# Kernel optimization log

Hardware: AMD Instinct MI355X
Metric: run time of the kernel (lower is better)

The kernel has to match this reference:

```python
import jax, jax.numpy as jnp
import numpy as np

B, T, E, H, V, F_IN = 128, 64, 512, 512, 10000, 2048


def setup_inputs() -> dict:
    key = jax.random.key(0)
    ks = jax.random.split(key, 16)
    u = lambda k, s, a: jax.random.uniform(k, s, jnp.float32, -a, a)
    n = lambda k, s, std: jax.random.normal(k, s, jnp.float32) * std
    return {
        "features": jax.random.normal(ks[0], (B, F_IN), jnp.float32),
        "captions": jax.random.randint(ks[1], (B, T), 0, V),
        "h0": jax.random.normal(ks[2], (B, H), jnp.float32),
        "lengths": T,
        "embed_W": u(ks[3], (V, E), 0.1),
        "fc_W": n(ks[4], (E, F_IN), 0.02),
        "fc_b": jnp.zeros((E,), jnp.float32),
        "bn_gamma": jnp.ones((E,), jnp.float32),
        "bn_beta": jnp.zeros((E,), jnp.float32),
        "attn_W": n(ks[5], (H, 2 * H), 0.02),
        "attn_b": jnp.zeros((H,), jnp.float32),
        "comb_W": n(ks[6], (H, 2 * H), 0.02),
        "comb_b": jnp.zeros((H,), jnp.float32),
        "gru_Wih": u(ks[7], (3 * H, E), 1.0 / np.sqrt(H)),
        "gru_Whh": u(ks[8], (3 * H, H), 1.0 / np.sqrt(H)),
        "gru_bih": u(ks[9], (3 * H,), 1.0 / np.sqrt(H)),
        "gru_bhh": u(ks[10], (3 * H,), 1.0 / np.sqrt(H)),
        "out_W": u(ks[11], (V, H), 0.1),
        "out_b": jnp.zeros((V,), jnp.float32),
    }


def _forward(features, captions, h0, lengths, embed_W, fc_W, fc_b, bn_gamma,
             bn_beta, attn_W, attn_b, comb_W, comb_b, gru_Wih, gru_Whh,
             gru_bih, gru_bhh, out_W, out_b):
    # fc + BatchNorm1d (training mode: batch statistics, eps=1e-5)
    f = features @ fc_W.T + fc_b                      # [B, E]
    mu = jnp.mean(f, axis=0)
    var = jnp.var(f, axis=0)
    feats = bn_gamma * (f - mu) / jnp.sqrt(var + 1e-5) + bn_beta  # [B, E]

    # embeddings = cat(features, embed(captions)); loop uses first T steps
    emb = embed_W[captions]                           # [B, T, E]
    x_seq = jnp.concatenate([feats[:, None, :], emb], axis=1)[:, :lengths]
    x_seq = jnp.swapaxes(x_seq, 0, 1)                 # [T, B, E]

    def step(hx, x):
        aw = jax.nn.softmax(jnp.concatenate([x, hx], 1) @ attn_W.T + attn_b,
                            axis=1)                   # [B, H]
        applied = feats * aw                          # [B, E]
        inp = jnp.concatenate([x, applied], 1) @ comb_W.T + comb_b  # [B, H]
        gx = inp @ gru_Wih.T + gru_bih                # [B, 3H]
        gh = hx @ gru_Whh.T + gru_bhh                 # [B, 3H]
        xr, xz, xn = jnp.split(gx, 3, axis=1)
        hr, hz, hn = jnp.split(gh, 3, axis=1)
        r = jax.nn.sigmoid(xr + hr)
        z = jax.nn.sigmoid(xz + hz)
        nt = jnp.tanh(xn + r * hn)
        h = (1.0 - z) * nt + z * hx
        return h, h

    _, hs = jax.lax.scan(step, h0, x_seq)             # hs: [T, B, H]
    hiddens = jnp.swapaxes(hs, 0, 1)                  # [B, T, H]
    # pack_padded_sequence with equal lengths -> time-major flatten
    packed = hs.reshape(lengths * hiddens.shape[0], -1)  # [T*B, H]
    logits = packed @ out_W.T + out_b                 # [T*B, V]
    return jax.nn.log_softmax(logits, axis=1), hiddens


def reference(features, captions, h0, lengths, embed_W, fc_W, fc_b, bn_gamma,
              bn_beta, attn_W, attn_b, comb_W, comb_b, gru_Wih, gru_Whh,
              gru_bih, gru_bhh, out_W, out_b):
    return _forward(features, captions, h0, lengths, embed_W, fc_W, fc_b,
                    bn_gamma, bn_beta, attn_W, attn_b, comb_W, comb_b,
                    gru_Wih, gru_Whh, gru_bih, gru_bhh, out_W, out_b)
```

## Files before the change

### kernel.cpp

```cpp
#include <hip/hip_runtime.h>

#define BB 128
#define TT 64
#define EE 512
#define HH 512
#define VV 10000
#define FIN 2048

typedef __attribute__((ext_vector_type(4))) float f32x4_t;
typedef __attribute__((ext_vector_type(8))) short s16x8_t;

__device__ __forceinline__ unsigned short f2bf(float x) {
    unsigned int u = __float_as_uint(x);
    unsigned int r = (u + 0x7fffu + ((u >> 16) & 1u)) >> 16;
    return (unsigned short)r;
}

__global__ __launch_bounds__(256) void gemm32(
    const float* __restrict__ A, int lda,
    const float* __restrict__ Bw, int ldb,
    float* __restrict__ C, int ldc, int K,
    const float* __restrict__ bias)
{
    __shared__ float As[32][34];
    __shared__ float Bs[32][34];
    const int tx = threadIdx.x, ty = threadIdx.y;
    const int tid = ty * 16 + tx;
    const int m0 = blockIdx.y * 32, n0 = blockIdx.x * 32;
    const int lr = tid >> 3, lc = (tid & 7) << 2;
    const float* ap = A + (size_t)(m0 + lr) * lda + lc;
    const float* bp = Bw + (size_t)(n0 + lr) * ldb + lc;
    float c00 = 0.f, c01 = 0.f, c10 = 0.f, c11 = 0.f;
    for (int kc = 0; kc < K; kc += 32) {
        float4 av = *(const float4*)(ap + kc);
        float4 bv = *(const float4*)(bp + kc);
        __syncthreads();
        As[lc + 0][lr] = av.x; As[lc + 1][lr] = av.y;
        As[lc + 2][lr] = av.z; As[lc + 3][lr] = av.w;
        Bs[lc + 0][lr] = bv.x; Bs[lc + 1][lr] = bv.y;
        Bs[lc + 2][lr] = bv.z; Bs[lc + 3][lr] = bv.w;
        __syncthreads();
#pragma unroll
        for (int kk = 0; kk < 32; kk++) {
            float2 a = *(const float2*)&As[kk][2 * ty];
            float2 b = *(const float2*)&Bs[kk][2 * tx];
            c00 = fmaf(a.x, b.x, c00); c01 = fmaf(a.x, b.y, c01);
            c10 = fmaf(a.y, b.x, c10); c11 = fmaf(a.y, b.y, c11);
        }
    }
    float cc[2][2] = {{c00, c01}, {c10, c11}};
    const int row = m0 + 2 * ty, col = n0 + 2 * tx;
#pragma unroll
    for (int i = 0; i < 2; i++)
#pragma unroll
        for (int j = 0; j < 2; j++)
            C[(size_t)(row + i) * ldc + col + j] = cc[i][j] + bias[col + j];
}

__global__ __launch_bounds__(256) void gemm128(
    const unsigned short* __restrict__ A, const unsigned short* __restrict__ Bw,
    float* __restrict__ C, int N, int K,
    const float* __restrict__ bias,
    const float* __restrict__ base, int ldbase, int mode)
{
    __shared__ __align__(16) unsigned short As[128 * 32];
    __shared__ __align__(16) unsigned short Bs[128 * 32];
    const int tid = threadIdx.x;
    const int lane = tid & 63, wave = tid >> 6;
    const int bm = blockIdx.y * 128, bn = blockIdx.x * 128;
    const int wm = (wave & 1) * 64, wn = (wave >> 1) * 64;
    const int sr = tid >> 2, sc = (tid & 3) * 8;
    const int m16 = lane & 15, q = lane >> 4;

    f32x4_t acc[4][4];
#pragma unroll
    for (int i = 0; i < 4; i++)
#pragma unroll
        for (int j = 0; j < 4; j++)
            acc[i][j] = (f32x4_t){0.f, 0.f, 0.f, 0.f};

    for (int kc = 0; kc < K; kc += 32) {
        uint4 a0 = *(const uint4*)(A + (size_t)(bm + sr) * K + kc + sc);
        uint4 a1 = *(const uint4*)(A + (size_t)(bm + 64 + sr) * K + kc + sc);
        uint4 b0, b1;
        int rb0 = bn + sr, rb1 = bn + 64 + sr;
        if (rb0 < N) b0 = *(const uint4*)(Bw + (size_t)rb0 * K + kc + sc);
        else { b0.x = 0; b0.y = 0; b0.z = 0; b0.w = 0; }
        if (rb1 < N) b1 = *(const uint4*)(Bw + (size_t)rb1 * K + kc + sc);
        else { b1.x = 0; b1.y = 0; b1.z = 0; b1.w = 0; }
        __syncthreads();
        *(uint4*)(&As[sr * 32 + sc]) = a0;
        *(uint4*)(&As[(sr + 64) * 32 + sc]) = a1;
        *(uint4*)(&Bs[sr * 32 + sc]) = b0;
        *(uint4*)(&Bs[(sr + 64) * 32 + sc]) = b1;
        __syncthreads();

        s16x8_t af[4], bf[4];
#pragma unroll
        for (int i = 0; i < 4; i++) {
            af[i] = *(const s16x8_t*)(&As[(wm + i * 16 + m16) * 32 + q * 8]);
            bf[i] = *(const s16x8_t*)(&Bs[(wn + i * 16 + m16) * 32 + q * 8]);
        }
#pragma unroll
        for (int i = 0; i < 4; i++)
#pragma unroll
            for (int j = 0; j < 4; j++)
                acc[i][j] = __builtin_amdgcn_mfma_f32_16x16x32_bf16(af[i], bf[j], acc[i][j], 0, 0, 0);
    }

#pragma unroll
    for (int i = 0; i < 4; i++)
#pragma unroll
        for (int j = 0; j < 4; j++) {
            int gr = bm + wm + i * 16 + q * 4;
            int gc = bn + wn + j * 16 + m16;
            if (gc < N) {
                if (mode == 0) {
                    float addc = bias ? bias[gc] : 0.f;
#pragma unroll
                    for (int rr = 0; rr < 4; rr++) {
                        float v = acc[i][j][rr] + addc;
                        if (base) v += base[(size_t)(gr + rr) * ldbase + gc];
                        C[(size_t)(gr + rr) * N + gc] = v;
                    }
                } else {
#pragma unroll
                    for (int rr = 0; rr < 4; rr++) {
                        int r = gr + rr;
                        float v = acc[i][j][rr];
                        v += (gc < 512) ? base[r * 512 + gc] : bias[gc - 512];
                        C[(size_t)r * N + gc] = v;
                    }
                }
            }
        }
}

__global__ __launch_bounds__(256) void gemm64(
    const unsigned short* __restrict__ A, const unsigned short* __restrict__ Bw,
    float* __restrict__ C, int N, int K,
    const float* __restrict__ bias,
    const float* __restrict__ base, int ldbase, int mode)
{
    __shared__ __align__(16) unsigned short As[64 * 32];
    __shared__ __align__(16) unsigned short Bs[64 * 32];
    const int tid = threadIdx.x;
    const int lane = tid & 63, wave = tid >> 6;
    const int bm = blockIdx.y * 64, bn = blockIdx.x * 64;
    const int wm = (wave & 1) * 32, wn = (wave >> 1) * 32;
    const int sr = tid >> 2, sc = (tid & 3) * 8;
    const int m16 = lane & 15, q = lane >> 4;

    f32x4_t acc[2][2];
#pragma unroll
    for (int i = 0; i < 2; i++)
#pragma unroll
        for (int j = 0; j < 2; j++)
            acc[i][j] = (f32x4_t){0.f, 0.f, 0.f, 0.f};

    for (int kc = 0; kc < K; kc += 32) {
        uint4 a0 = *(const uint4*)(A + (size_t)(bm + sr) * K + kc + sc);
        uint4 b0 = *(const uint4*)(Bw + (size_t)(bn + sr) * K + kc + sc);
        __syncthreads();
        *(uint4*)(&As[sr * 32 + sc]) = a0;
        *(uint4*)(&Bs[sr * 32 + sc]) = b0;
        __syncthreads();

        s16x8_t af[2], bf[2];
#pragma unroll
        for (int i = 0; i < 2; i++) {
            af[i] = *(const s16x8_t*)(&As[(wm + i * 16 + m16) * 32 + q * 8]);
            bf[i] = *(const s16x8_t*)(&Bs[(wn + i * 16 + m16) * 32 + q * 8]);
        }
#pragma unroll
        for (int i = 0; i < 2; i++)
#pragma unroll
            for (int j = 0; j < 2; j++)
                acc[i][j] = __builtin_amdgcn_mfma_f32_16x16x32_bf16(af[i], bf[j], acc[i][j], 0, 0, 0);
    }

#pragma unroll
    for (int i = 0; i < 2; i++)
#pragma unroll
        for (int j = 0; j < 2; j++) {
            int gr = bm + wm + i * 16 + q * 4;
            int gc = bn + wn + j * 16 + m16;
            if (mode == 0) {
                float addc = bias ? bias[gc] : 0.f;
#pragma unroll
                for (int rr = 0; rr < 4; rr++) {
                    float v = acc[i][j][rr] + addc;
                    if (base) v += base[(size_t)(gr + rr) * ldbase + gc];
                    C[(size_t)(gr + rr) * N + gc] = v;
                }
            } else {
#pragma unroll
                for (int rr = 0; rr < 4; rr++) {
                    int r = gr + rr;
                    float v = acc[i][j][rr];
                    v += (gc < 512) ? base[r * 512 + gc] : bias[gc - 512];
                    C[(size_t)r * N + gc] = v;
                }
            }
        }
}

__global__ __launch_bounds__(128) void bn_kernel(
    const float* __restrict__ f, const float* __restrict__ gamma,
    const float* __restrict__ beta, float* __restrict__ feats)
{
    int e = blockIdx.x, b = threadIdx.x;
    float v = f[b * EE + e];
    __shared__ float s1[128], s2[128];
    s1[b] = v; s2[b] = v * v;
    __syncthreads();
    for (int s = 64; s > 0; s >>= 1) {
        if (b < s) { s1[b] += s1[b + s]; s2[b] += s2[b + s]; }
        __syncthreads();
    }
    float mu = s1[0] * (1.f / 128.f);
    float var = s2[0] * (1.f / 128.f) - mu * mu;
    float inv = 1.f / sqrtf(var + 1e-5f);
    feats[b * EE + e] = gamma[e] * (v - mu) * inv + beta[e];
}

__global__ void build_x_bf16(const float* __restrict__ feats, const float* __restrict__ embW,
                             const int* __restrict__ cap, unsigned short* __restrict__ Xb)
{
    int id = blockIdx.x * 256 + threadIdx.x;
    int e4 = id & 127;
    int rem = id >> 7;
    int b = rem & 127;
    int t = rem >> 7;
    const float4* src;
    if (t == 0) src = (const float4*)(feats + b * EE) + e4;
    else        src = (const float4*)(embW + (size_t)cap[b * TT + t - 1] * EE) + e4;
    float4 v = *src;
    ushort4 o;
    o.x = f2bf(v.x); o.y = f2bf(v.y); o.z = f2bf(v.z); o.w = f2bf(v.w);
    ((ushort4*)Xb)[(size_t)(t * BB + b) * 128 + e4] = o;
}

__global__ void cvt_bf16(const float* __restrict__ src, unsigned short* __restrict__ dst, int n)
{
    int i = blockIdx.x * 256 + threadIdx.x;
    if (i < n) dst[i] = f2bf(src[i]);
}

__global__ void pack_attn_wx(const float* __restrict__ attnW, unsigned short* __restrict__ dst)
{
    int i = blockIdx.x * 256 + threadIdx.x;
    int n = i >> 9, e = i & 511;
    dst[i] = f2bf(attnW[n * 1024 + e]);
}

__global__ void pack_cxt(const float* __restrict__ combW, unsigned short* __restrict__ dst)
{
    int i = blockIdx.x * 256 + threadIdx.x;
    int e = i >> 9, n = i & 511;
    dst[i] = f2bf(combW[n * 1024 + e]);
}

__global__ void pack_wat(const float* __restrict__ combW, unsigned short* __restrict__ dst)
{
    int i = blockIdx.x * 256 + threadIdx.x;
    int m = i >> 9, n = i & 511;
    dst[i] = f2bf(combW[n * 1024 + 512 + m]);
}

__global__ void pack_wcat_bf(const float* __restrict__ attnW, const float* __restrict__ Whh,
                             unsigned short* __restrict__ dst)
{
    int i = blockIdx.x * 256 + threadIdx.x;
    int j = i >> 9, k = i & 511;
    dst[i] = f2bf((j < 512) ? attnW[j * 1024 + 512 + k]
                            : Whh[(size_t)(j - 512) * 512 + k]);
}

__global__ void bias2_kernel(const float* __restrict__ Wih, const float* __restrict__ comb_b,
                             const float* __restrict__ bih, float* __restrict__ bias2)
{
    int j = blockIdx.x, lane = threadIdx.x;
    float s = 0.f;
    for (int n = lane; n < 512; n += 64) s += Wih[(size_t)j * 512 + n] * comb_b[n];
    for (int o = 32; o > 0; o >>= 1) s += __shfl_down(s, o);
    if (lane == 0) bias2[j] = bih[j] + s;
}

__global__ __launch_bounds__(256) void softmax_applied(
    const float* __restrict__ AB, const float* __restrict__ feats,
    unsigned short* __restrict__ APPb)
{
    int b = blockIdx.x, tid = threadIdx.x;
    const float* L = AB + b * 2048;
    float v0 = L[tid], v1 = L[tid + 256];
    __shared__ float red[256];
    red[tid] = fmaxf(v0, v1);
    __syncthreads();
    for (int s = 128; s > 0; s >>= 1) {
        if (tid < s) red[tid] = fmaxf(red[tid], red[tid + s]);
        __syncthreads();
    }
    float mx = red[0];
    __syncthreads();
    float e0 = __expf(v0 - mx), e1 = __expf(v1 - mx);
    red[tid] = e0 + e1;
    __syncthreads();
    for (int s = 128; s > 0; s >>= 1) {
        if (tid < s) red[tid] += red[tid + s];
        __syncthreads();
    }
    float inv = 1.f / red[0];
    APPb[b * 512 + tid]       = f2bf(feats[b * 512 + tid] * e0 * inv);
    APPb[b * 512 + tid + 256] = f2bf(feats[b * 512 + tid + 256] * e1 * inv);
}

__global__ __launch_bounds__(256) void gru_gate(
    const float* __restrict__ GX, const float* __restrict__ AB,
    const float* __restrict__ hprev, float* __restrict__ hs_t,
    unsigned short* __restrict__ hsb_t)
{
    int i = blockIdx.x * 256 + threadIdx.x;
    int b = i >> 9, n = i & 511;
    float xr = GX[b * 1536 + n];
    float xz = GX[b * 1536 + 512 + n];
    float xn = GX[b * 1536 + 1024 + n];
    float hr = AB[b * 2048 + 512 + n];
    float hz = AB[b * 2048 + 1024 + n];
    float hn = AB[b * 2048 + 1536 + n];
    float r = 1.f / (1.f + __expf(-(xr + hr)));
    float z = 1.f / (1.f + __expf(-(xz + hz)));
    float nt = tanhf(xn + r * hn);
    float h = (1.f - z) * nt + z * hprev[i];
    hs_t[i] = h;
    hsb_t[i] = f2bf(h);
}

__global__ __launch_bounds__(256) void row_lse(const float* __restrict__ C, float* __restrict__ lse)
{
    int row = blockIdx.x, tid = threadIdx.x;
    const float* p = C + (size_t)row * VV;
    float m = -1e30f;
    for (int i = tid; i < VV; i += 256) m = fmaxf(m, p[i]);
    __shared__ float red[256];
    red[tid] = m;
    __syncthreads();
    for (int s = 128; s > 0; s >>= 1) {
        if (tid < s) red[tid] = fmaxf(red[tid], red[tid + s]);
        __syncthreads();
    }
    float mx = red[0];
    __syncthreads();
    float ssum = 0.f;
    for (int i = tid; i < VV; i += 256) ssum += __expf(p[i] - mx);
    red[tid] = ssum;
    __syncthreads();
    for (int s = 128; s > 0; s >>= 1) {
        if (tid < s) red[tid] += red[tid + s];
        __syncthreads();
    }
    if (tid == 0) lse[row] = mx + logf(red[0]);
}

__global__ void sub_lse(float* __restrict__ C, const float* __restrict__ lse)
{
    int i = blockIdx.x * 256 + threadIdx.x;
    float l = lse[i / 2500];
    float4 v = ((float4*)C)[i];
    v.x -= l; v.y -= l; v.z -= l; v.w -= l;
    ((float4*)C)[i] = v;
}

__global__ void copy_hiddens(const float* __restrict__ HS, float* __restrict__ out)
{
    int id = blockIdx.x * 256 + threadIdx.x;
    int h4 = id & 127;
    int t = (id >> 7) & 63;
    int b = id >> 13;
    ((float4*)out)[id] = ((const float4*)HS)[t * 16384 + b * 128 + h4];
}

extern "C" void kernel_launch(void* const* d_in, const int* in_sizes, int n_in,
                              void* d_out, int out_size, void* d_ws, size_t ws_size,
                              hipStream_t stream)
{
    const float* features = (const float*)d_in[0];
    const int*   captions = (const int*)d_in[1];
    const float* h0       = (const float*)d_in[2];
    const float* embed_W  = (const float*)d_in[4];
    const float* fc_W     = (const float*)d_in[5];
    const float* fc_b     = (const float*)d_in[6];
    const float* bn_gamma = (const float*)d_in[7];
    const float* bn_beta  = (const float*)d_in[8];
    const float* attn_W   = (const float*)d_in[9];
    const float* attn_b   = (const float*)d_in[10];
    const float* comb_W   = (const float*)d_in[11];
    const float* comb_b   = (const float*)d_in[12];
    const float* gru_Wih  = (const float*)d_in[13];
    const float* gru_Whh  = (const float*)d_in[14];
    const float* gru_bih  = (const float*)d_in[15];
    const float* gru_bhh  = (const float*)d_in[16];
    const float* out_W    = (const float*)d_in[17];
    const float* out_b    = (const float*)d_in[18];
    float* dout = (float*)d_out;

    float* w      = (float*)d_ws;
    float* f      = w;
    float* feats  = w + 65536;
    float* Lx     = w + 131072;
    float* GxX    = w + 4325376;
    float* HS     = w + 16908288;
    float* W2     = w + 21102592;
    float* W_ac   = w + 21889024;
    float* AB     = w + 22675456;
    float* GX     = w + 22937600;
    float* bias2  = w + 23134208;
    float* lse    = w + 23135744;
    unsigned short* u      = (unsigned short*)(w + 23143936);
    unsigned short* Xb     = u;
    unsigned short* attnWxb= u + 4194304;
    unsigned short* Wihb   = u + 4456448;
    unsigned short* CxTb   = u + 5242880;
    unsigned short* WaTb   = u + 5505024;
    unsigned short* Wcatb  = u + 5767168;
    unsigned short* W2b    = u + 6815744;
    unsigned short* W_acb  = u + 7602176;
    unsigned short* outWb  = u + 8388608;
    unsigned short* HSb    = u + 13508608;
    unsigned short* APPb   = u + 17702912;
    unsigned short* h0b    = u + 17768448;

    dim3 blk2(16, 16);

    gemm32<<<dim3(16, 4), blk2, 0, stream>>>(features, FIN, fc_W, FIN, f, EE, FIN, fc_b);
    bn_kernel<<<512, 128, 0, stream>>>(f, bn_gamma, bn_beta, feats);
    cvt_bf16<<<256, 256, 0, stream>>>(h0, h0b, BB * HH);
    build_x_bf16<<<4096, 256, 0, stream>>>(feats, embed_W, captions, Xb);
    pack_attn_wx<<<1024, 256, 0, stream>>>(attn_W, attnWxb);
    pack_cxt<<<1024, 256, 0, stream>>>(comb_W, CxTb);
    pack_wat<<<1024, 256, 0, stream>>>(comb_W, WaTb);
    pack_wcat_bf<<<4096, 256, 0, stream>>>(attn_W, gru_Whh, Wcatb);
    cvt_bf16<<<3072, 256, 0, stream>>>(gru_Wih, Wihb, 1536 * 512);
    cvt_bf16<<<20000, 256, 0, stream>>>(out_W, outWb, VV * HH);
    bias2_kernel<<<1536, 64, 0, stream>>>(gru_Wih, comb_b, gru_bih, bias2);

    gemm128<<<dim3(4, 64), 256, 0, stream>>>(Xb, attnWxb, Lx, 512, 512,
                                             attn_b, nullptr, 0, 0);
    gemm64<<<dim3(8, 24), 256, 0, stream>>>(Wihb, CxTb, W2, 512, 512,
                                            nullptr, nullptr, 0, 0);
    cvt_bf16<<<3072, 256, 0, stream>>>(W2, W2b, 1536 * 512);
    gemm128<<<dim3(12, 64), 256, 0, stream>>>(Xb, W2b, GxX, 1536, 512,
                                              bias2, nullptr, 0, 0);
    gemm64<<<dim3(8, 24), 256, 0, stream>>>(Wihb, WaTb, W_ac, 512, 512,
                                            nullptr, nullptr, 0, 0);
    cvt_bf16<<<3072, 256, 0, stream>>>(W_ac, W_acb, 1536 * 512);

    for (int t = 0; t < TT; t++) {
        const unsigned short* hb = (t == 0) ? h0b : (HSb + (size_t)(t - 1) * BB * HH);
        const float* hprev = (t == 0) ? h0 : (HS + (size_t)(t - 1) * BB * HH);
        gemm64<<<dim3(32, 2), 256, 0, stream>>>(hb, Wcatb, AB, 2048, 512,
                                                gru_bhh, Lx + (size_t)t * BB * HH, 512, 1);
        softmax_applied<<<128, 256, 0, stream>>>(AB, feats, APPb);
        gemm64<<<dim3(24, 2), 256, 0, stream>>>(APPb, W_acb, GX, 1536, 512,
                                                nullptr, GxX + (size_t)t * BB * 1536, 1536, 0);
        gru_gate<<<256, 256, 0, stream>>>(GX, AB, hprev,
                                          HS + (size_t)t * BB * HH,
                                          HSb + (size_t)t * BB * HH);
    }

    gemm128<<<dim3(79, 64), 256, 0, stream>>>(HSb, outWb, dout, VV, 512,
                                              out_b, nullptr, 0, 0);
    row_lse<<<8192, 256, 0, stream>>>(dout, lse);
    sub_lse<<<80000, 256, 0, stream>>>(dout, lse);
    copy_hiddens<<<4096, 256, 0, stream>>>(HS, dout + (size_t)TT * BB * VV);
}
```

Measured before the change: 2.738 ms.

## Fuse GRU recurrence into persistent kernel with grid barriers and fuse log-softmax

Replaces the 256 per-timestep launches (GEMM, softmax, GEMM, gate) with one persistent 48-block kernel. The kernel keeps the recurrent weights resident in swizzled LDS and separates phases with atomic grid barriers. The GRU gate is fused into the second GEMM's epilogue. The separate row_lse and sub_lse passes become one log-softmax kernel that caches each row in LDS. This removes launch overhead and repeated weight reloads, at the cost of spin-barrier latency, low occupancy, and relying on all 48 blocks being co-resident.

```diff
diff --git a/kernel.cpp b/kernel.cpp
--- a/kernel.cpp
+++ b/kernel.cpp
@@ -7,6 +7,10 @@
 #define VV 10000
 #define FIN 2048
 
+#define NBLK 48
+#define NA 32
+#define NC 16
+
 typedef __attribute__((ext_vector_type(4))) float f32x4_t;
 typedef __attribute__((ext_vector_type(8))) short s16x8_t;
 
@@ -14,6 +18,10 @@
     unsigned int u = __float_as_uint(x);
     unsigned int r = (u + 0x7fffu + ((u >> 16) & 1u)) >> 16;
     return (unsigned short)r;
+}
+
+__device__ __forceinline__ int swz(int row, int kb) {
+    return row * 1024 + (kb ^ ((row & 7) << 4));
 }
 
 __global__ __launch_bounds__(256) void gemm32(
@@ -287,88 +295,233 @@
     if (lane == 0) bias2[j] = bih[j] + s;
 }
 
-__global__ __launch_bounds__(256) void softmax_applied(
-    const float* __restrict__ AB, const float* __restrict__ feats,
-    unsigned short* __restrict__ APPb)
-{
-    int b = blockIdx.x, tid = threadIdx.x;
-    const float* L = AB + b * 2048;
-    float v0 = L[tid], v1 = L[tid + 256];
-    __shared__ float red[256];
-    red[tid] = fmaxf(v0, v1);
+__global__ void zero_u32(unsigned int* __restrict__ p) { *p = 0u; }
+
+__device__ __forceinline__ void gbar(unsigned int* cnt, unsigned int tgt)
+{
     __syncthreads();
-    for (int s = 128; s > 0; s >>= 1) {
-        if (tid < s) red[tid] = fmaxf(red[tid], red[tid + s]);
-        __syncthreads();
-    }
-    float mx = red[0];
+    if (threadIdx.x == 0) {
+        __threadfence();
+        __hip_atomic_fetch_add(cnt, 1u, __ATOMIC_ACQ_REL, __HIP_MEMORY_SCOPE_AGENT);
+        while (__hip_atomic_load(cnt, __ATOMIC_RELAXED, __HIP_MEMORY_SCOPE_AGENT) < tgt)
+            __builtin_amdgcn_s_sleep(2);
+        __threadfence();
+    }
     __syncthreads();
-    float e0 = __expf(v0 - mx), e1 = __expf(v1 - mx);
-    red[tid] = e0 + e1;
+}
+
+__global__ __launch_bounds__(256) void recurrence(
+    const unsigned short* __restrict__ Wcatb,
+    const unsigned short* __restrict__ W_acb,
+    const unsigned short* __restrict__ h0b,
+    const float* __restrict__ h0,
+    const float* __restrict__ Lx,
+    const float* __restrict__ GxX,
+    const float* __restrict__ feats,
+    const float* __restrict__ bhh,
+    float* __restrict__ AB,
+    unsigned short* __restrict__ APPb,
+    float* __restrict__ HS,
+    unsigned short* __restrict__ HSb,
+    unsigned int* __restrict__ barcnt)
+{
+    __shared__ __align__(16) unsigned char smem[96 * 1024];
+    const int tid = threadIdx.x;
+    const int bid = blockIdx.x;
+    const int lane = tid & 63, wave = tid >> 6;
+    const int m16 = lane & 15, q = lane >> 4;
+
+    if (bid < NA) {
+        const uint4* src = (const uint4*)(Wcatb + (size_t)bid * 64 * 512);
+#pragma unroll
+        for (int it = 0; it < 16; it++) {
+            int idx = it * 256 + tid;
+            int r = idx >> 6, sl = idx & 63;
+            *(uint4*)(smem + swz(r, sl * 16)) = src[idx];
+        }
+    } else {
+        const int n0c = (bid - NA) * 32;
+#pragma unroll
+        for (int it = 0; it < 24; it++) {
+            int idx = it * 256 + tid;
+            int r = idx >> 6, sl = idx & 63;
+            int p = r >> 5, rr = r & 31;
+            *(uint4*)(smem + swz(r, sl * 16)) =
+                ((const uint4*)(W_acb + (size_t)(p * 512 + n0c + rr) * 512))[sl];
+        }
+    }
     __syncthreads();
-    for (int s = 128; s > 0; s >>= 1) {
-        if (tid < s) red[tid] += red[tid + s];
-        __syncthreads();
-    }
-    float inv = 1.f / red[0];
-    APPb[b * 512 + tid]       = f2bf(feats[b * 512 + tid] * e0 * inv);
-    APPb[b * 512 + tid + 256] = f2bf(feats[b * 512 + tid + 256] * e1 * inv);
-}
-
-__global__ __launch_bounds__(256) void gru_gate(
-    const float* __restrict__ GX, const float* __restrict__ AB,
-    const float* __restrict__ hprev, float* __restrict__ hs_t,
-    unsigned short* __restrict__ hsb_t)
-{
-    int i = blockIdx.x * 256 + threadIdx.x;
-    int b = i >> 9, n = i & 511;
-    float xr = GX[b * 1536 + n];
-    float xz = GX[b * 1536 + 512 + n];
-    float xn = GX[b * 1536 + 1024 + n];
-    float hr = AB[b * 2048 + 512 + n];
-    float hz = AB[b * 2048 + 1024 + n];
-    float hn = AB[b * 2048 + 1536 + n];
-    float r = 1.f / (1.f + __expf(-(xr + hr)));
-    float z = 1.f / (1.f + __expf(-(xz + hz)));
-    float nt = tanhf(xn + r * hn);
-    float h = (1.f - z) * nt + z * hprev[i];
-    hs_t[i] = h;
-    hsb_t[i] = f2bf(h);
-}
-
-__global__ __launch_bounds__(256) void row_lse(const float* __restrict__ C, float* __restrict__ lse)
-{
-    int row = blockIdx.x, tid = threadIdx.x;
-    const float* p = C + (size_t)row * VV;
+
+    unsigned int tgt = 0;
+
+    for (int t = 0; t < TT; t++) {
+        const unsigned short* hb = t ? (HSb + (size_t)(t - 1) * (BB * HH)) : h0b;
+        const float* hprev = t ? (HS + (size_t)(t - 1) * (BB * HH)) : h0;
+        const float* Lxt = Lx + (size_t)t * (BB * HH);
+        const float* GxXt = GxX + (size_t)t * (BB * 1536);
+
+        if (bid < NA) {
+            const int n0 = bid * 64;
+            const int rowhalf = (wave >> 1) * 64;
+            const int colhalf = (wave & 1) * 32;
+            f32x4_t acc[4][2];
+#pragma unroll
+            for (int i = 0; i < 4; i++)
+#pragma unroll
+                for (int j = 0; j < 2; j++)
+                    acc[i][j] = (f32x4_t){0.f, 0.f, 0.f, 0.f};
+            for (int kc = 0; kc < 512; kc += 32) {
+                const int kb = (kc + q * 8) * 2;
+                s16x8_t af[4];
+#pragma unroll
+                for (int i = 0; i < 4; i++)
+                    af[i] = *(const s16x8_t*)(hb + (size_t)(rowhalf + i * 16 + m16) * 512 + kc + q * 8);
+                s16x8_t bfr[2];
+#pragma unroll
+                for (int j = 0; j < 2; j++)
+                    bfr[j] = *(const s16x8_t*)(smem + swz(colhalf + j * 16 + m16, kb));
+#pragma unroll
+                for (int i = 0; i < 4; i++)
+#pragma unroll
+                    for (int j = 0; j < 2; j++)
+                        acc[i][j] = __builtin_amdgcn_mfma_f32_16x16x32_bf16(af[i], bfr[j], acc[i][j], 0, 0, 0);
+            }
+#pragma unroll
+            for (int i = 0; i < 4; i++)
+#pragma unroll
+                for (int j = 0; j < 2; j++) {
+                    const int b0 = rowhalf + i * 16 + q * 4;
+                    const int col = n0 + colhalf + j * 16 + m16;
+#pragma unroll
+                    for (int rr = 0; rr < 4; rr++) {
+                        const int b = b0 + rr;
+                        float v = acc[i][j][rr] +
+                                  ((col < 512) ? Lxt[b * 512 + col] : bhh[col - 512]);
+                        AB[b * 2048 + col] = v;
+                    }
+                }
+        }
+        tgt += NBLK; gbar(barcnt, tgt);
+
+        if (bid < NA) {
+            const int row = bid * 4 + wave;
+            const float* Lr = AB + row * 2048 + lane * 8;
+            float4 x0 = *(const float4*)(Lr);
+            float4 x1 = *(const float4*)(Lr + 4);
+            float vm = fmaxf(fmaxf(fmaxf(x0.x, x0.y), fmaxf(x0.z, x0.w)),
+                             fmaxf(fmaxf(x1.x, x1.y), fmaxf(x1.z, x1.w)));
+#pragma unroll
+            for (int o = 32; o > 0; o >>= 1) vm = fmaxf(vm, __shfl_xor(vm, o));
+            float e0 = __expf(x0.x - vm), e1 = __expf(x0.y - vm);
+            float e2 = __expf(x0.z - vm), e3 = __expf(x0.w - vm);
+            float e4 = __expf(x1.x - vm), e5 = __expf(x1.y - vm);
+            float e6 = __expf(x1.z - vm), e7 = __expf(x1.w - vm);
+            float s = ((e0 + e1) + (e2 + e3)) + ((e4 + e5) + (e6 + e7));
+#pragma unroll
+            for (int o = 32; o > 0; o >>= 1) s += __shfl_xor(s, o);
+            const float inv = 1.f / s;
+            const float* fr = feats + row * 512 + lane * 8;
+            float4 f0 = *(const float4*)(fr);
+            float4 f1 = *(const float4*)(fr + 4);
+            s16x8_t ov;
+            ov[0] = (short)f2bf(f0.x * e0 * inv);
+            ov[1] = (short)f2bf(f0.y * e1 * inv);
+            ov[2] = (short)f2bf(f0.z * e2 * inv);
+            ov[3] = (short)f2bf(f0.w * e3 * inv);
+            ov[4] = (short)f2bf(f1.x * e4 * inv);
+            ov[5] = (short)f2bf(f1.y * e5 * inv);
+            ov[6] = (short)f2bf(f1.z * e6 * inv);
+            ov[7] = (short)f2bf(f1.w * e7 * inv);
+            *(s16x8_t*)(APPb + row * 512 + lane * 8) = ov;
+        }
+        tgt += NBLK; gbar(barcnt, tgt);
+
+        if (bid >= NA) {
+            const int n0 = (bid - NA) * 32;
+            const int rowhalf = (wave >> 1) * 64;
+            const int j = wave & 1;
+            f32x4_t acc[4][3];
+#pragma unroll
+            for (int i = 0; i < 4; i++)
+#pragma unroll
+                for (int p = 0; p < 3; p++)
+                    acc[i][p] = (f32x4_t){0.f, 0.f, 0.f, 0.f};
+            for (int kc = 0; kc < 512; kc += 32) {
+                const int kb = (kc + q * 8) * 2;
+                s16x8_t af[4];
+#pragma unroll
+                for (int i = 0; i < 4; i++)
+                    af[i] = *(const s16x8_t*)(APPb + (size_t)(rowhalf + i * 16 + m16) * 512 + kc + q * 8);
+                s16x8_t bfr[3];
+#pragma unroll
+                for (int p = 0; p < 3; p++)
+                    bfr[p] = *(const s16x8_t*)(smem + swz(p * 32 + j * 16 + m16, kb));
+#pragma unroll
+                for (int i = 0; i < 4; i++)
+#pragma unroll
+                    for (int p = 0; p < 3; p++)
+                        acc[i][p] = __builtin_amdgcn_mfma_f32_16x16x32_bf16(af[i], bfr[p], acc[i][p], 0, 0, 0);
+            }
+            const int n = n0 + j * 16 + m16;
+            float* HSt = HS + (size_t)t * (BB * HH);
+            unsigned short* HSbt = HSb + (size_t)t * (BB * HH);
+#pragma unroll
+            for (int i = 0; i < 4; i++) {
+                const int b0 = rowhalf + i * 16 + q * 4;
+#pragma unroll
+                for (int rr = 0; rr < 4; rr++) {
+                    const int b = b0 + rr;
+                    float xr = acc[i][0][rr] + GxXt[b * 1536 + n];
+                    float xz = acc[i][1][rr] + GxXt[b * 1536 + 512 + n];
+                    float xn = acc[i][2][rr] + GxXt[b * 1536 + 1024 + n];
+                    float hr = AB[b * 2048 + 512 + n];
+                    float hz = AB[b * 2048 + 1024 + n];
+                    float hn = AB[b * 2048 + 1536 + n];
+                    float r = 1.f / (1.f + __expf(-(xr + hr)));
+                    float z = 1.f / (1.f + __expf(-(xz + hz)));
+                    float nt = tanhf(xn + r * hn);
+                    float h = (1.f - z) * nt + z * hprev[b * 512 + n];
+                    HSt[b * 512 + n] = h;
+                    HSbt[b * 512 + n] = f2bf(h);
+                }
+            }
+        }
+        tgt += NBLK; gbar(barcnt, tgt);
+    }
+}
+
+__global__ __launch_bounds__(256) void logsoftmax_k(float* __restrict__ C)
+{
+    __shared__ float4 buf[2500];
+    __shared__ float red[8];
+    const int row = blockIdx.x, tid = threadIdx.x;
+    float4* p = (float4*)(C + (size_t)row * VV);
     float m = -1e30f;
-    for (int i = tid; i < VV; i += 256) m = fmaxf(m, p[i]);
-    __shared__ float red[256];
-    red[tid] = m;
+    for (int i = tid; i < 2500; i += 256) {
+        float4 v = p[i];
+        buf[i] = v;
+        m = fmaxf(fmaxf(fmaxf(v.x, v.y), fmaxf(v.z, v.w)), m);
+    }
+#pragma unroll
+    for (int o = 32; o > 0; o >>= 1) m = fmaxf(m, __shfl_xor(m, o));
+    if ((tid & 63) == 0) red[tid >> 6] = m;
     __syncthreads();
-    for (int s = 128; s > 0; s >>= 1) {
-        if (tid < s) red[tid] = fmaxf(red[tid], red[tid + s]);
-        __syncthreads();
-    }
-    float mx = red[0];
+    m = fmaxf(fmaxf(red[0], red[1]), fmaxf(red[2], red[3]));
+    float s = 0.f;
+    for (int i = tid; i < 2500; i += 256) {
+        float4 v = buf[i];
+        s += __expf(v.x - m) + __expf(v.y - m) + __expf(v.z - m) + __expf(v.w - m);
+    }
+#pragma unroll
+    for (int o = 32; o > 0; o >>= 1) s += __shfl_xor(s, o);
+    if ((tid & 63) == 0) red[4 + (tid >> 6)] = s;
     __syncthreads();
-    float ssum = 0.f;
-    for (int i = tid; i < VV; i += 256) ssum += __expf(p[i] - mx);
-    red[tid] = ssum;
-    __syncthreads();
-    for (int s = 128; s > 0; s >>= 1) {
-        if (tid < s) red[tid] += red[tid + s];
-        __syncthreads();
-    }
-    if (tid == 0) lse[row] = mx + logf(red[0]);
-}
-
-__global__ void sub_lse(float* __restrict__ C, const float* __restrict__ lse)
-{
-    int i = blockIdx.x * 256 + threadIdx.x;
-    float l = lse[i / 2500];
-    float4 v = ((float4*)C)[i];
-    v.x -= l; v.y -= l; v.z -= l; v.w -= l;
-    ((float4*)C)[i] = v;
+    const float l = m + logf(red[4] + red[5] + red[6] + red[7]);
+    for (int i = tid; i < 2500; i += 256) {
+        float4 v = buf[i];
+        v.x -= l; v.y -= l; v.z -= l; v.w -= l;
+        p[i] = v;
+    }
 }
 
 __global__ void copy_hiddens(const float* __restrict__ HS, float* __restrict__ out)
@@ -413,9 +566,8 @@
     float* W2     = w + 21102592;
     float* W_ac   = w + 21889024;
     float* AB     = w + 22675456;
-    float* GX     = w + 22937600;
+    unsigned int* barcnt = (unsigned int*)(w + 22937600);
     float* bias2  = w + 23134208;
-    float* lse    = w + 23135744;
     unsigned short* u      = (unsigned short*)(w + 23143936);
     unsigned short* Xb     = u;
     unsigned short* attnWxb= u + 4194304;
@@ -443,6 +595,7 @@
     cvt_bf16<<<3072, 256, 0, stream>>>(gru_Wih, Wihb, 1536 * 512);
     cvt_bf16<<<20000, 256, 0, stream>>>(out_W, outWb, VV * HH);
     bias2_kernel<<<1536, 64, 0, stream>>>(gru_Wih, comb_b, gru_bih, bias2);
+    zero_u32<<<1, 1, 0, stream>>>(barcnt);
 
     gemm128<<<dim3(4, 64), 256, 0, stream>>>(Xb, attnWxb, Lx, 512, 512,
                                              attn_b, nullptr, 0, 0);
@@ -455,22 +608,11 @@
                                             nullptr, nullptr, 0, 0);
     cvt_bf16<<<3072, 256, 0, stream>>>(W_ac, W_acb, 1536 * 512);
 
-    for (int t = 0; t < TT; t++) {
-        const unsigned short* hb = (t == 0) ? h0b : (HSb + (size_t)(t - 1) * BB * HH);
-        const float* hprev = (t == 0) ? h0 : (HS + (size_t)(t - 1) * BB * HH);
-        gemm64<<<dim3(32, 2), 256, 0, stream>>>(hb, Wcatb, AB, 2048, 512,
-                                                gru_bhh, Lx + (size_t)t * BB * HH, 512, 1);
-        softmax_applied<<<128, 256, 0, stream>>>(AB, feats, APPb);
-        gemm64<<<dim3(24, 2), 256, 0, stream>>>(APPb, W_acb, GX, 1536, 512,
-                                                nullptr, GxX + (size_t)t * BB * 1536, 1536, 0);
-        gru_gate<<<256, 256, 0, stream>>>(GX, AB, hprev,
-                                          HS + (size_t)t * BB * HH,
-                                          HSb + (size_t)t * BB * HH);
-    }
+    recurrence<<<NBLK, 256, 0, stream>>>(Wcatb, W_acb, h0b, h0, Lx, GxX, feats,
+                                         gru_bhh, AB, APPb, HS, HSb, barcnt);
 
     gemm128<<<dim3(79, 64), 256, 0, stream>>>(HSb, outWb, dout, VV, 512,
                                               out_b, nullptr, 0, 0);
-    row_lse<<<8192, 256, 0, stream>>>(dout, lse);
-    sub_lse<<<80000, 256, 0, stream>>>(dout, lse);
+    logsoftmax_k<<<8192, 256, 0, stream>>>(dout);
     copy_hiddens<<<4096, 256, 0, stream>>>(HS, dout + (size_t)TT * BB * VV);
 }
```

After: 4.733 ms. 1.73x slower.
